# Kernel optimization log

Hardware: AMD Instinct MI355X
Metric: run time of the kernel (lower is better)

The kernel has to match this reference:

```python
import jax, jax.numpy as jnp
import numpy as np

NUM_HEADS = 8
NEG_LARGE = -1e9  # stands in for -inf under the causal mask; masked entries get exactly 0 entmax weight


def _entmax15(z):
    """Exact 1.5-entmax along the last axis (Peters & Martins 2019 sort-based algorithm)."""
    z = z * 0.5
    zs = -jnp.sort(-z, axis=-1)                      # descending sort
    T = z.shape[-1]
    k = jnp.arange(1, T + 1, dtype=z.dtype)
    mean = jnp.cumsum(zs, axis=-1) / k
    mean_sq = jnp.cumsum(zs * zs, axis=-1) / k
    ss = k * (mean_sq - mean * mean)
    delta = (1.0 - ss) / k
    tau = mean - jnp.sqrt(jnp.maximum(delta, 0.0))
    support = jnp.sum(tau <= zs, axis=-1, keepdims=True)      # support size >= 1
    tau_star = jnp.take_along_axis(tau, support - 1, axis=-1)
    return jnp.square(jnp.maximum(z - tau_star, 0.0))


def setup_inputs() -> dict:
    key = jax.random.key(0)
    ks = jax.random.split(key, 9)
    B, T, D, H = 2, 2048, 512, NUM_HEADS
    dk = D // H
    s = 1.0 / np.sqrt(D)
    so = 1.0 / np.sqrt(dk)
    x = jax.random.normal(ks[0], (B, T, D), jnp.float32)
    Wq = jax.random.uniform(ks[1], (D, D), jnp.float32, -s, s)
    bq = jax.random.uniform(ks[2], (D,), jnp.float32, -s, s)
    Wk = jax.random.uniform(ks[3], (D, D), jnp.float32, -s, s)
    bk = jax.random.uniform(ks[4], (D,), jnp.float32, -s, s)
    Wv = jax.random.uniform(ks[5], (D, D), jnp.float32, -s, s)
    bv = jax.random.uniform(ks[6], (D,), jnp.float32, -s, s)
    Wo = jax.random.uniform(ks[7], (dk, D), jnp.float32, -so, so)
    bo = jax.random.uniform(ks[8], (D,), jnp.float32, -so, so)
    return {"x": x, "Wq": Wq, "bq": bq, "Wk": Wk, "bk": bk, "Wv": Wv, "bv": bv, "Wo": Wo, "bo": bo}


def reference(x, Wq, bq, Wk, bk, Wv, bv, Wo, bo):
    B, T, D = x.shape
    H = NUM_HEADS
    dk = D // H
    Q = (x @ Wq + bq).reshape(B, T, H, dk).transpose(0, 2, 1, 3)   # [B,H,T,dk]
    K = (x @ Wk + bk).reshape(B, T, H, dk).transpose(0, 2, 1, 3)
    V = (x @ Wv + bv).reshape(B, T, H, dk).transpose(0, 2, 1, 3)
    scores = jnp.einsum('bhtd,bhsd->bhts', Q, K) / np.float32(np.sqrt(dk))
    causal = jnp.triu(jnp.ones((T, T), bool), k=1)                 # True above diagonal
    scores = jnp.where(causal[None, None, :, :], jnp.float32(NEG_LARGE), scores)
    weights = _entmax15(scores)                                    # [B,H,T,T]
    weights_avg = weights.mean(axis=1)                             # [B,T,T]
    V_combined = V.mean(axis=1)                                    # [B,T,dk]
    out = jnp.einsum('bts,bsd->btd', weights_avg, V_combined)      # [B,T,dk]
    return out @ Wo + bo, weights_avg
```

## Files before the change

### kernel.cpp

```cpp
#include <hip/hip_runtime.h>
#include <hip/hip_bf16.h>
#include <cstdint>

#define B_ 2
#define T_ 2048
#define D_ 512
#define H_ 8
#define DK_ 64
#define TQ_ 4
#define NTL_ (T_ / TQ_)
#define M_ (B_ * T_)

#define SSC_ 8192.0f
#define S2_  (SSC_ * SSC_)

__global__ __launch_bounds__(256) void gemm_bias_kernel(
    const float* __restrict__ A, const float* __restrict__ W,
    const float* __restrict__ bias, float* __restrict__ C,
    int M, int N, int K)
{
  __shared__ float As[32][68];
  __shared__ float Bs[32][68];
  const int bm = blockIdx.y * 64;
  const int bn = blockIdx.x * 64;
  const int tid = threadIdx.x;
  const int tx = tid & 15, ty = tid >> 4;
  float acc[4][4] = {};
  for (int k0 = 0; k0 < K; k0 += 32) {
    {
      const int r = tid >> 2;
      const int c = (tid & 3) << 2;
      const float4 a0 = *reinterpret_cast<const float4*>(&A[(size_t)(bm + r) * K + k0 + c]);
      const float4 a1 = *reinterpret_cast<const float4*>(&A[(size_t)(bm + r) * K + k0 + 16 + c]);
      As[c + 0][r] = a0.x;  As[c + 1][r] = a0.y;  As[c + 2][r] = a0.z;  As[c + 3][r] = a0.w;
      As[c + 16][r] = a1.x; As[c + 17][r] = a1.y; As[c + 18][r] = a1.z; As[c + 19][r] = a1.w;
    }
    {
      const int r = tid >> 4;
      const int c = (tid & 15) << 2;
      *reinterpret_cast<float4*>(&Bs[r][c]) =
          *reinterpret_cast<const float4*>(&W[(size_t)(k0 + r) * N + bn + c]);
      *reinterpret_cast<float4*>(&Bs[r + 16][c]) =
          *reinterpret_cast<const float4*>(&W[(size_t)(k0 + 16 + r) * N + bn + c]);
    }
    __syncthreads();
#pragma unroll
    for (int kk = 0; kk < 32; ++kk) {
      const float4 av = *reinterpret_cast<const float4*>(&As[kk][ty * 4]);
      const float4 bv = *reinterpret_cast<const float4*>(&Bs[kk][tx * 4]);
      acc[0][0] = fmaf(av.x, bv.x, acc[0][0]); acc[0][1] = fmaf(av.x, bv.y, acc[0][1]);
      acc[0][2] = fmaf(av.x, bv.z, acc[0][2]); acc[0][3] = fmaf(av.x, bv.w, acc[0][3]);
      acc[1][0] = fmaf(av.y, bv.x, acc[1][0]); acc[1][1] = fmaf(av.y, bv.y, acc[1][1]);
      acc[1][2] = fmaf(av.y, bv.z, acc[1][2]); acc[1][3] = fmaf(av.y, bv.w, acc[1][3]);
      acc[2][0] = fmaf(av.z, bv.x, acc[2][0]); acc[2][1] = fmaf(av.z, bv.y, acc[2][1]);
      acc[2][2] = fmaf(av.z, bv.z, acc[2][2]); acc[2][3] = fmaf(av.z, bv.w, acc[2][3]);
      acc[3][0] = fmaf(av.w, bv.x, acc[3][0]); acc[3][1] = fmaf(av.w, bv.y, acc[3][1]);
      acc[3][2] = fmaf(av.w, bv.z, acc[3][2]); acc[3][3] = fmaf(av.w, bv.w, acc[3][3]);
    }
    __syncthreads();
  }
#pragma unroll
  for (int i = 0; i < 4; ++i) {
    const int row = bm + ty * 4 + i;
#pragma unroll
    for (int j = 0; j < 4; ++j) {
      const int col = bn + tx * 4 + j;
      C[(size_t)row * N + col] = acc[i][j] + bias[col];
    }
  }
}

__global__ __launch_bounds__(256) void gemm_bias_kernelT(
    const float* __restrict__ A, const float* __restrict__ W,
    const float* __restrict__ bias, float* __restrict__ Ct,
    int M, int N, int K)
{
  __shared__ float As[32][68];
  __shared__ float Bs[32][68];
  const int bm = blockIdx.y * 64;
  const int bn = blockIdx.x * 64;
  const int tid = threadIdx.x;
  const int tx = tid & 15, ty = tid >> 4;
  float acc[4][4] = {};
  for (int k0 = 0; k0 < K; k0 += 32) {
    {
      const int r = tid >> 2;
      const int c = (tid & 3) << 2;
      const float4 a0 = *reinterpret_cast<const float4*>(&A[(size_t)(bm + r) * K + k0 + c]);
      const float4 a1 = *reinterpret_cast<const float4*>(&A[(size_t)(bm + r) * K + k0 + 16 + c]);
      As[c + 0][r] = a0.x;  As[c + 1][r] = a0.y;  As[c + 2][r] = a0.z;  As[c + 3][r] = a0.w;
      As[c + 16][r] = a1.x; As[c + 17][r] = a1.y; As[c + 18][r] = a1.z; As[c + 19][r] = a1.w;
    }
    {
      const int r = tid >> 4;
      const int c = (tid & 15) << 2;
      *reinterpret_cast<float4*>(&Bs[r][c]) =
          *reinterpret_cast<const float4*>(&W[(size_t)(k0 + r) * N + bn + c]);
      *reinterpret_cast<float4*>(&Bs[r + 16][c]) =
          *reinterpret_cast<const float4*>(&W[(size_t)(k0 + 16 + r) * N + bn + c]);
    }
    __syncthreads();
#pragma unroll
    for (int kk = 0; kk < 32; ++kk) {
      const float4 av = *reinterpret_cast<const float4*>(&As[kk][ty * 4]);
      const float4 bv = *reinterpret_cast<const float4*>(&Bs[kk][tx * 4]);
      acc[0][0] = fmaf(av.x, bv.x, acc[0][0]); acc[0][1] = fmaf(av.x, bv.y, acc[0][1]);
      acc[0][2] = fmaf(av.x, bv.z, acc[0][2]); acc[0][3] = fmaf(av.x, bv.w, acc[0][3]);
      acc[1][0] = fmaf(av.y, bv.x, acc[1][0]); acc[1][1] = fmaf(av.y, bv.y, acc[1][1]);
      acc[1][2] = fmaf(av.y, bv.z, acc[1][2]); acc[1][3] = fmaf(av.y, bv.w, acc[1][3]);
      acc[2][0] = fmaf(av.z, bv.x, acc[2][0]); acc[2][1] = fmaf(av.z, bv.y, acc[2][1]);
      acc[2][2] = fmaf(av.z, bv.z, acc[2][2]); acc[2][3] = fmaf(av.z, bv.w, acc[2][3]);
      acc[3][0] = fmaf(av.w, bv.x, acc[3][0]); acc[3][1] = fmaf(av.w, bv.y, acc[3][1]);
      acc[3][2] = fmaf(av.w, bv.z, acc[3][2]); acc[3][3] = fmaf(av.w, bv.w, acc[3][3]);
    }
    __syncthreads();
  }
#pragma unroll
  for (int j = 0; j < 4; ++j) {
    const int col = bn + tx * 4 + j;
    const float bb = bias[col];
    const float4 v = make_float4(acc[0][j] + bb, acc[1][j] + bb, acc[2][j] + bb, acc[3][j] + bb);
    *reinterpret_cast<float4*>(&Ct[(size_t)col * M + bm + ty * 4]) = v;
  }
}

__global__ __launch_bounds__(256) void vcombine_kernel(const float* __restrict__ V,
                                                       float* __restrict__ Vc)
{
  const int idx = blockIdx.x * 256 + threadIdx.x;
  if (idx >= M_ * DK_) return;
  const int row = idx >> 6, d = idx & 63;
  float s = 0.f;
#pragma unroll
  for (int h = 0; h < H_; ++h) s += V[(size_t)row * D_ + h * DK_ + d];
  Vc[idx] = s * 0.125f;
}

__global__ __launch_bounds__(256) void zero_kernel(float4* __restrict__ p, int n4)
{
  const int stride = gridDim.x * 256;
  const float4 z = make_float4(0.f, 0.f, 0.f, 0.f);
  for (int i = blockIdx.x * 256 + threadIdx.x; i < n4; i += stride) p[i] = z;
}

__global__ __launch_bounds__(256, 6)
void attn_kernel(
    const float* __restrict__ Qg, const float* __restrict__ Kt,
    float* __restrict__ wavg)
{
  __shared__ short ssc[TQ_][T_];

  const int tid = threadIdx.x;
  const int bid = blockIdx.x;
  const int h = bid >> 10;
  const int b = (bid >> 9) & 1;
  const int tile = (NTL_ - 1) - (bid & 511);
  const int t0 = tile * TQ_;
  const int nS = t0 + TQ_;
  const int wave = __builtin_amdgcn_readfirstlane(tid >> 6);
  const int lane = tid & 63;

  {
    const float* Qp = &Qg[(size_t)(b * T_ + t0) * D_ + h * DK_];
#pragma unroll 1
    for (int c = 0; c < T_; c += 1024) {
      if (c < nS) {
        const int s0 = min(tid * 4 + c, nS - 4);
        const float* Ktp = &Kt[(size_t)(h * DK_) * M_ + b * T_ + s0];
        float4 a[TQ_];
#pragma unroll
        for (int r = 0; r < TQ_; ++r) a[r] = make_float4(0.f, 0.f, 0.f, 0.f);
#pragma unroll 2
        for (int d4 = 0; d4 < 16; ++d4) {
          const float4 k0 = *reinterpret_cast<const float4*>(Ktp + (size_t)(d4 * 4 + 0) * M_);
          const float4 k1 = *reinterpret_cast<const float4*>(Ktp + (size_t)(d4 * 4 + 1) * M_);
          const float4 k2 = *reinterpret_cast<const float4*>(Ktp + (size_t)(d4 * 4 + 2) * M_);
          const float4 k3 = *reinterpret_cast<const float4*>(Ktp + (size_t)(d4 * 4 + 3) * M_);
#pragma unroll
          for (int r = 0; r < TQ_; ++r) {
            const float q0 = Qp[r * D_ + d4 * 4 + 0];
            const float q1 = Qp[r * D_ + d4 * 4 + 1];
            const float q2 = Qp[r * D_ + d4 * 4 + 2];
            const float q3 = Qp[r * D_ + d4 * 4 + 3];
            a[r].x = fmaf(q0, k0.x, a[r].x); a[r].y = fmaf(q0, k0.y, a[r].y);
            a[r].z = fmaf(q0, k0.z, a[r].z); a[r].w = fmaf(q0, k0.w, a[r].w);
            a[r].x = fmaf(q1, k1.x, a[r].x); a[r].y = fmaf(q1, k1.y, a[r].y);
            a[r].z = fmaf(q1, k1.z, a[r].z); a[r].w = fmaf(q1, k1.w, a[r].w);
            a[r].x = fmaf(q2, k2.x, a[r].x); a[r].y = fmaf(q2, k2.y, a[r].y);
            a[r].z = fmaf(q2, k2.z, a[r].z); a[r].w = fmaf(q2, k2.w, a[r].w);
            a[r].x = fmaf(q3, k3.x, a[r].x); a[r].y = fmaf(q3, k3.y, a[r].y);
            a[r].z = fmaf(q3, k3.z, a[r].z); a[r].w = fmaf(q3, k3.w, a[r].w);
          }
        }
#pragma unroll
        for (int r = 0; r < TQ_; ++r) {
          const int i0 = __float2int_rn(fminf(fmaxf(a[r].x * 512.f, -32000.f), 32000.f));
          const int i1 = __float2int_rn(fminf(fmaxf(a[r].y * 512.f, -32000.f), 32000.f));
          const int i2 = __float2int_rn(fminf(fmaxf(a[r].z * 512.f, -32000.f), 32000.f));
          const int i3 = __float2int_rn(fminf(fmaxf(a[r].w * 512.f, -32000.f), 32000.f));
          short4 st; st.x = (short)i0; st.y = (short)i1; st.z = (short)i2; st.w = (short)i3;
          *reinterpret_cast<short4*>(&ssc[r][s0]) = st;
        }
      }
    }
  }
  __syncthreads();

  const int t = t0 + wave;
  const int n = t + 1;
  float srow[32];

#pragma unroll
  for (int j = 0; j < 4; ++j) {
    if (j * 512 < n) {
      const uint4 pk = *reinterpret_cast<const uint4*>(&ssc[wave][j * 512 + lane * 8]);
      const unsigned pw[4] = {pk.x, pk.y, pk.z, pk.w};
#pragma unroll
      for (int q = 0; q < 4; ++q) {
        const int s_lo = j * 512 + lane * 8 + q * 2;
        const float lo = (float)((int)(short)(pw[q] & 0xffffu));
        const float hi = (float)((int)pw[q] >> 16);
        srow[j * 8 + q * 2 + 0] = (s_lo + 0 < n) ? lo : -1e30f;
        srow[j * 8 + q * 2 + 1] = (s_lo + 1 < n) ? hi : -1e30f;
      }
    } else {
#pragma unroll
      for (int q = 0; q < 8; ++q) srow[j * 8 + q] = -1e30f;
    }
  }
  asm volatile("" ::: "memory");

  float mx = -1e30f;
#pragma unroll
  for (int i = 0; i < 32; ++i) mx = fmaxf(mx, srow[i]);
#pragma unroll
  for (int m = 32; m >= 1; m >>= 1) mx = fmaxf(mx, __shfl_xor(mx, m, 64));

  float tau = mx - SSC_;
#pragma unroll 1
  for (int it = 0; it < 12; ++it) {
    float s1 = 0.f, s2 = 0.f, cn = 0.f;
#pragma unroll
    for (int j = 0; j < 4; ++j) {
      if (j * 512 < n) {
#pragma unroll
        for (int q = 0; q < 8; ++q) {
          const float u = fmaxf(srow[j * 8 + q] - tau, 0.f);
          s1 += u;
          s2 = fmaf(u, u, s2);
          cn += (u > 0.f) ? 1.f : 0.f;
        }
      }
    }
#pragma unroll
    for (int m = 32; m >= 1; m >>= 1) {
      s1 += __shfl_xor(s1, m, 64);
      s2 += __shfl_xor(s2, m, 64);
    }
    if (fabsf(s2 - S2_) < 672.f) break;
    if (it < 3) {
#pragma unroll
      for (int m = 32; m >= 1; m >>= 1) cn += __shfl_xor(cn, m, 64);
      const float kf = fmaxf(cn, 1.f);
      const float mu = tau + s1 / kf;
      const float ss = s2 - s1 * s1 / kf;
      tau = mu - sqrtf(fmaxf((S2_ - ss) / kf, 0.f));
    } else {
      tau += (s2 - S2_) / fmaxf(2.f * s1, 1e-6f);
    }
  }
  tau = fminf(tau, mx - 1.f);

  const float wconv = 0.125f / (SSC_ * SSC_);
  float* const wrow = &wavg[(size_t)(b * T_ + t) * T_];
#pragma unroll
  for (int j = 0; j < 4; ++j) {
    if (j * 512 < n) {
#pragma unroll
      for (int q = 0; q < 8; ++q) {
        const float u = fmaxf(srow[j * 8 + q] - tau, 0.f);
        if (__any(u > 0.f)) {
          if (u > 0.f) {
            const int s = j * 512 + lane * 8 + q;
            atomicAdd(&wrow[s], u * u * wconv);
          }
        }
      }
    }
  }
}

__global__ __launch_bounds__(256) void pv_kernel(
    const float* __restrict__ wavg, const float* __restrict__ Vc,
    float* __restrict__ AO)
{
  __shared__ float part[4][DK_];
  const int row = blockIdx.x;
  const int b = row >> 11;
  const int t = row & (T_ - 1);
  const int wave = __builtin_amdgcn_readfirstlane(threadIdx.x >> 6);
  const int lane = threadIdx.x & 63;
  const int n = t + 1;
  const float* wr = &wavg[(size_t)row * T_];
  const float* vb = &Vc[(size_t)(b * T_) * DK_ + lane];
  float acc = 0.f;
#pragma unroll 1
  for (int s0 = wave * 4; s0 < n; s0 += 16) {
    const float4 w4 = *reinterpret_cast<const float4*>(&wr[s0]);
    const unsigned nz = __float_as_uint(w4.x) | __float_as_uint(w4.y) |
                        __float_as_uint(w4.z) | __float_as_uint(w4.w);
    if (__builtin_amdgcn_readfirstlane(nz) != 0u) {
      acc = fmaf(w4.x, vb[(size_t)(s0 + 0) * DK_], acc);
      acc = fmaf(w4.y, vb[(size_t)(s0 + 1) * DK_], acc);
      acc = fmaf(w4.z, vb[(size_t)(s0 + 2) * DK_], acc);
      acc = fmaf(w4.w, vb[(size_t)(s0 + 3) * DK_], acc);
    }
  }
  part[wave][lane] = acc;
  __syncthreads();
  if (wave == 0) {
    AO[(size_t)row * DK_ + lane] =
        part[0][lane] + part[1][lane] + part[2][lane] + part[3][lane];
  }
}

extern "C" void kernel_launch(void* const* d_in, const int* in_sizes, int n_in,
                              void* d_out, int out_size, void* d_ws, size_t ws_size,
                              hipStream_t stream)
{
  const float* x  = (const float*)d_in[0];
  const float* Wq = (const float*)d_in[1];
  const float* bq = (const float*)d_in[2];
  const float* Wk = (const float*)d_in[3];
  const float* bk = (const float*)d_in[4];
  const float* Wv = (const float*)d_in[5];
  const float* bv = (const float*)d_in[6];
  const float* Wo = (const float*)d_in[7];
  const float* bo = (const float*)d_in[8];
  float* out = (float*)d_out;
  float* ws  = (float*)d_ws;

  float* Q  = ws;
  float* Kt = Q + (size_t)M_ * D_;
  float* V  = Kt + (size_t)D_ * M_;
  float* Vc = V + (size_t)M_ * D_;
  float* AO = Vc + (size_t)M_ * DK_;

  float* out1 = out;
  float* wavg = out + (size_t)M_ * D_;

  const dim3 gp(D_ / 64, M_ / 64);
  gemm_bias_kernel <<<gp, 256, 0, stream>>>(x, Wq, bq, Q,  M_, D_, D_);
  gemm_bias_kernelT<<<gp, 256, 0, stream>>>(x, Wk, bk, Kt, M_, D_, D_);
  gemm_bias_kernel <<<gp, 256, 0, stream>>>(x, Wv, bv, V,  M_, D_, D_);
  vcombine_kernel<<<(M_ * DK_ + 255) / 256, 256, 0, stream>>>(V, Vc);

  zero_kernel<<<2048, 256, 0, stream>>>(reinterpret_cast<float4*>(wavg),
                                        (int)((size_t)B_ * T_ * T_ / 4));

  attn_kernel<<<H_ * B_ * NTL_, 256, 0, stream>>>(Q, Kt, wavg);
  pv_kernel<<<M_, 256, 0, stream>>>(wavg, Vc, AO);
  gemm_bias_kernel<<<gp, 256, 0, stream>>>(AO, Wo, bo, out1, M_, D_, DK_);
}
```

Measured before the change: 386.2 us.

## Fuse PV product into attention kernel with per-head partials and reduce

The attention kernel now computes each row's weighted sum over V_combined directly from the entmax weights. It walks the ballot mask of nonzero weights and broadcasts each weight with a shuffle. Per-head partial outputs go to a scratch buffer that reuses the V region, and a small reduce kernel sums them over heads. This removes the separate pv_kernel, which re-read the full dense weight matrix, at the cost of a serial per-nonzero loop and extra V loads inside the attention kernel. The score-tile bounds check also changed from clamping s0 to skipping out-of-range threads.

Measured after the change: 381.1 us. No clear change (-1.3%).

```diff
diff --git a/kernel.cpp b/kernel.cpp
--- a/kernel.cpp
+++ b/kernel.cpp
@@ -146,7 +146,8 @@
 __global__ __launch_bounds__(256, 6)
 void attn_kernel(
     const float* __restrict__ Qg, const float* __restrict__ Kt,
-    float* __restrict__ wavg)
+    const float* __restrict__ Vc, float* __restrict__ wavg,
+    float* __restrict__ AOh)
 {
   __shared__ short ssc[TQ_][T_];
 
@@ -164,8 +165,8 @@
     const float* Qp = &Qg[(size_t)(b * T_ + t0) * D_ + h * DK_];
 #pragma unroll 1
     for (int c = 0; c < T_; c += 1024) {
-      if (c < nS) {
-        const int s0 = min(tid * 4 + c, nS - 4);
+      const int s0 = tid * 4 + c;
+      if (s0 < nS) {
         const float* Ktp = &Kt[(size_t)(h * DK_) * M_ + b * T_ + s0];
         float4 a[TQ_];
 #pragma unroll
@@ -273,55 +274,43 @@
 
   const float wconv = 0.125f / (SSC_ * SSC_);
   float* const wrow = &wavg[(size_t)(b * T_ + t) * T_];
+  const float* const vb = &Vc[(size_t)(b * T_) * DK_ + lane];
+  float pv = 0.f;
 #pragma unroll
   for (int j = 0; j < 4; ++j) {
     if (j * 512 < n) {
 #pragma unroll
       for (int q = 0; q < 8; ++q) {
         const float u = fmaxf(srow[j * 8 + q] - tau, 0.f);
-        if (__any(u > 0.f)) {
-          if (u > 0.f) {
-            const int s = j * 512 + lane * 8 + q;
-            atomicAdd(&wrow[s], u * u * wconv);
+        const float w2 = u * u;
+        unsigned long long mask = __ballot(w2 > 0.f);
+        if (mask) {
+          if (w2 > 0.f) {
+            atomicAdd(&wrow[j * 512 + lane * 8 + q], w2 * wconv);
+          }
+          while (mask) {
+            const int l = (int)__ffsll((unsigned long long)mask) - 1;
+            mask &= mask - 1;
+            const float wl = __shfl(w2, l, 64);
+            const int sl = j * 512 + l * 8 + q;
+            pv = fmaf(wl, vb[(size_t)sl * DK_], pv);
           }
         }
       }
     }
   }
-}
-
-__global__ __launch_bounds__(256) void pv_kernel(
-    const float* __restrict__ wavg, const float* __restrict__ Vc,
-    float* __restrict__ AO)
-{
-  __shared__ float part[4][DK_];
-  const int row = blockIdx.x;
-  const int b = row >> 11;
-  const int t = row & (T_ - 1);
-  const int wave = __builtin_amdgcn_readfirstlane(threadIdx.x >> 6);
-  const int lane = threadIdx.x & 63;
-  const int n = t + 1;
-  const float* wr = &wavg[(size_t)row * T_];
-  const float* vb = &Vc[(size_t)(b * T_) * DK_ + lane];
-  float acc = 0.f;
-#pragma unroll 1
-  for (int s0 = wave * 4; s0 < n; s0 += 16) {
-    const float4 w4 = *reinterpret_cast<const float4*>(&wr[s0]);
-    const unsigned nz = __float_as_uint(w4.x) | __float_as_uint(w4.y) |
-                        __float_as_uint(w4.z) | __float_as_uint(w4.w);
-    if (__builtin_amdgcn_readfirstlane(nz) != 0u) {
-      acc = fmaf(w4.x, vb[(size_t)(s0 + 0) * DK_], acc);
-      acc = fmaf(w4.y, vb[(size_t)(s0 + 1) * DK_], acc);
-      acc = fmaf(w4.z, vb[(size_t)(s0 + 2) * DK_], acc);
-      acc = fmaf(w4.w, vb[(size_t)(s0 + 3) * DK_], acc);
-    }
-  }
-  part[wave][lane] = acc;
-  __syncthreads();
-  if (wave == 0) {
-    AO[(size_t)row * DK_ + lane] =
-        part[0][lane] + part[1][lane] + part[2][lane] + part[3][lane];
-  }
+  AOh[((size_t)h * M_ + b * T_ + t) * DK_ + lane] = pv * wconv;
+}
+
+__global__ __launch_bounds__(256) void aoreduce_kernel(
+    const float* __restrict__ AOh, float* __restrict__ AO)
+{
+  const int idx = blockIdx.x * 256 + threadIdx.x;
+  if (idx >= M_ * DK_) return;
+  float s = 0.f;
+#pragma unroll
+  for (int h = 0; h < H_; ++h) s += AOh[(size_t)h * M_ * DK_ + idx];
+  AO[idx] = s;
 }
 
 extern "C" void kernel_launch(void* const* d_in, const int* in_sizes, int n_in,
@@ -340,11 +329,12 @@
   float* out = (float*)d_out;
   float* ws  = (float*)d_ws;
 
-  float* Q  = ws;
-  float* Kt = Q + (size_t)M_ * D_;
-  float* V  = Kt + (size_t)D_ * M_;
-  float* Vc = V + (size_t)M_ * D_;
-  float* AO = Vc + (size_t)M_ * DK_;
+  float* Q   = ws;
+  float* Kt  = Q + (size_t)M_ * D_;
+  float* V   = Kt + (size_t)D_ * M_;
+  float* Vc  = V + (size_t)M_ * D_;
+  float* AO  = Vc + (size_t)M_ * DK_;
+  float* AOh = V;
 
   float* out1 = out;
   float* wavg = out + (size_t)M_ * D_;
@@ -358,7 +348,7 @@
   zero_kernel<<<2048, 256, 0, stream>>>(reinterpret_cast<float4*>(wavg),
                                         (int)((size_t)B_ * T_ * T_ / 4));
 
-  attn_kernel<<<H_ * B_ * NTL_, 256, 0, stream>>>(Q, Kt, wavg);
-  pv_kernel<<<M_, 256, 0, stream>>>(wavg, Vc, AO);
+  attn_kernel<<<H_ * B_ * NTL_, 256, 0, stream>>>(Q, Kt, Vc, wavg, AOh);
+  aoreduce_kernel<<<(M_ * DK_ + 255) / 256, 256, 0, stream>>>(AOh, AO);
   gemm_bias_kernel<<<gp, 256, 0, stream>>>(AO, Wo, bo, out1, M_, D_, DK_);
 }
```
